# Kernel tuning notes

Hardware: AMD Instinct MI355X
Metric: run time of the kernel (lower is better)

The kernel has to match this reference:

```python
import jax, jax.numpy as jnp
import numpy as np

NS, NI, NC, C, E, M = 50000, 20000, 1000, 128, 1000000, 250000


def setup_inputs() -> dict:
    key = jax.random.key(0)
    ks = jax.random.split(key, 12)
    xavier = (2.0 / (C + C)) ** 0.5  # xavier_normal_ std for square weight
    return {
        "stu_x": jax.random.normal(ks[0], (NS, C), jnp.float32),
        "item_x": jax.random.normal(ks[1], (NI, C), jnp.float32),
        "conc_x": jax.random.normal(ks[2], (NC, C), jnp.float32),
        "W_stu": jax.random.normal(ks[3], (C, C), jnp.float32) * xavier,
        "b_stu": jnp.zeros((C,), jnp.float32),
        "W_item": jax.random.normal(ks[4], (C, C), jnp.float32) * xavier,
        "b_item": jnp.zeros((C,), jnp.float32),
        "W_pred": jax.random.normal(ks[5], (1, C), jnp.float32) * ((2.0 / (1 + C)) ** 0.5),
        "b_pred": jnp.zeros((1,), jnp.float32),
        "stu_track": jax.random.randint(ks[6], (E,), 0, NS, jnp.int32),
        "item_index": jax.random.randint(ks[7], (E,), 0, NI, jnp.int32),
        "conc_index": jax.random.randint(ks[8], (E,), 0, NC, jnp.int32),
        "mean_index": jax.random.randint(ks[9], (E,), 0, M, jnp.int32),
        "num_segments": M,
    }


def _segment_mean(vals, seg_ids, num_segments):
    sums = jax.ops.segment_sum(vals, seg_ids, num_segments=num_segments)
    cnt = jax.ops.segment_sum(jnp.ones((vals.shape[0], 1), vals.dtype), seg_ids,
                              num_segments=num_segments)
    return sums / jnp.maximum(cnt, 1.0)


def reference(stu_x, item_x, conc_x, W_stu, b_stu, W_item, b_item, W_pred, b_pred,
              stu_track, item_index, conc_index, mean_index, num_segments):
    # Feature (stu): shared lin_l=lin_r; aggregate is identity -> per-edge output
    conc_s = conc_x @ W_stu.T          # [NC, C] projected source (concepts)
    stu_p = stu_x @ W_stu.T            # [NS, C] projected target (students)
    stu_feature = jax.nn.sigmoid(conc_s[conc_index] + stu_p[stu_track] + b_stu)  # [E, C]

    # Feature (item): SparseTensor(row=item, col=conc) -> x_j from conc, x_i from item
    conc_i = conc_x @ W_item.T         # [NC, C]
    item_p = item_x @ W_item.T         # [NI, C]
    item_feature = jax.nn.sigmoid(conc_i[conc_index] + item_p[item_index] + b_item)  # [E, C]

    # scatter-mean of per-edge difference over mean_index groups
    pred_input = _segment_mean(stu_feature - item_feature, mean_index, num_segments)  # [M, C]
    pred = jax.nn.sigmoid(pred_input @ W_pred.T + b_pred)  # [M, 1]
    return pred.reshape(-1)
```

## Files before the change

kernel.cpp:

```cpp
#include <hip/hip_runtime.h>

typedef unsigned short u16;
typedef unsigned int   u32;

typedef short short8 __attribute__((ext_vector_type(8)));
typedef float floatx4 __attribute__((ext_vector_type(4)));

#define CDIM 128
#define K_NEG_LOG2E -1.4426950408889634f
#define CNT_SCALE 16777216.0

__device__ __forceinline__ float bf2f_lo(u32 h) {
    union { u32 u; float f; } v; v.u = h << 16; return v.f;
}
__device__ __forceinline__ float bf2f_hi(u32 h) {
    union { u32 u; float f; } v; v.u = h & 0xffff0000u; return v.f;
}
__device__ __forceinline__ u16 f2bf(float f) {
    union { float f; u32 u; } v; v.f = f;
    u32 u = v.u;
    return (u16)((u + 0x7FFFu + ((u >> 16) & 1u)) >> 16);
}
__device__ __forceinline__ float sig_std(float x) {
    return __builtin_amdgcn_rcpf(1.0f + __builtin_amdgcn_exp2f(x * K_NEG_LOG2E));
}

__global__ __launch_bounds__(256) void prep_kernel(
    const float* __restrict__ Wstu, const float* __restrict__ Witem,
    u32* __restrict__ Wbf_pair, float4* __restrict__ zero4, int nZero4)
{
    const int tid = blockIdx.x * blockDim.x + threadIdx.x;
    const int stride = gridDim.x * blockDim.x;
    for (int i = tid; i < 16384; i += stride) {
        const float* W = (i & 8192) ? (Witem - 16384) : Wstu;
        const int j = i * 2;
        u32 lo = f2bf(W[j]     * K_NEG_LOG2E);
        u32 hi = f2bf(W[j + 1] * K_NEG_LOG2E);
        Wbf_pair[i] = lo | (hi << 16);
    }
    const float4 z = {0.f, 0.f, 0.f, 0.f};
    for (int i = tid; i < nZero4; i += stride) zero4[i] = z;
}

__device__ __forceinline__ void proj_tile32(
    const float* __restrict__ X, const u16* __restrict__ Wbf,
    const float* __restrict__ bias, u16* __restrict__ out,
    int nrows, int ostride, int ooff, int row0, int lane)
{
    const int m = lane & 15;
    const int g = lane >> 4;

    short8 a[2][4];
#pragma unroll
    for (int t = 0; t < 2; ++t) {
        int arow = row0 + t * 16 + m;
        if (arow >= nrows) arow = nrows - 1;
        const float* xrow = X + (size_t)arow * CDIM;
#pragma unroll
        for (int s = 0; s < 4; ++s) {
            float4 f0 = *(const float4*)(xrow + s * 32 + g * 8);
            float4 f1 = *(const float4*)(xrow + s * 32 + g * 8 + 4);
            a[t][s][0] = (short)f2bf(f0.x); a[t][s][1] = (short)f2bf(f0.y);
            a[t][s][2] = (short)f2bf(f0.z); a[t][s][3] = (short)f2bf(f0.w);
            a[t][s][4] = (short)f2bf(f1.x); a[t][s][5] = (short)f2bf(f1.y);
            a[t][s][6] = (short)f2bf(f1.z); a[t][s][7] = (short)f2bf(f1.w);
        }
    }

#pragma unroll
    for (int ct = 0; ct < 8; ++ct) {
        const u16* wrow = Wbf + (size_t)(ct * 16 + m) * CDIM;
        floatx4 acc0 = {0.f, 0.f, 0.f, 0.f};
        floatx4 acc1 = {0.f, 0.f, 0.f, 0.f};
#pragma unroll
        for (int s = 0; s < 4; ++s) {
            short8 b = *(const short8*)(wrow + s * 32 + g * 8);
            acc0 = __builtin_amdgcn_mfma_f32_16x16x32_bf16(a[0][s], b, acc0, 0, 0, 0);
            acc1 = __builtin_amdgcn_mfma_f32_16x16x32_bf16(a[1][s], b, acc1, 0, 0, 0);
        }
        const int col = ct * 16 + m;
        const float badd = bias ? bias[col] * K_NEG_LOG2E : 0.f;
#pragma unroll
        for (int i = 0; i < 4; ++i) {
            int r0 = row0 + g * 4 + i;
            if (r0 < nrows)
                out[(size_t)r0 * ostride + ooff + col] =
                    f2bf(__builtin_amdgcn_exp2f(acc0[i] + badd));
            int r1 = r0 + 16;
            if (r1 < nrows)
                out[(size_t)r1 * ostride + ooff + col] =
                    f2bf(__builtin_amdgcn_exp2f(acc1[i] + badd));
        }
    }
}

__global__ __launch_bounds__(256) void proj4_kernel(
    const float* __restrict__ stu_x, const float* __restrict__ item_x,
    const float* __restrict__ conc_x,
    const u16* __restrict__ Wstu_bf, const u16* __restrict__ Witem_bf,
    const float* __restrict__ b_stu, const float* __restrict__ b_item,
    u16* __restrict__ stu_p, u16* __restrict__ item_p, u16* __restrict__ conc_cat,
    int NS, int NI, int NC)
{
    const int lane = threadIdx.x & 63;
    int w = blockIdx.x * 4 + (threadIdx.x >> 6);
    const int T0 = (NS + 31) / 32, T1 = (NI + 31) / 32, T2 = (NC + 31) / 32;

    if (w < T0) { proj_tile32(stu_x, Wstu_bf, nullptr, stu_p, NS, 128, 0, w * 32, lane); return; }
    w -= T0;
    if (w < T1) { proj_tile32(item_x, Witem_bf, nullptr, item_p, NI, 128, 0, w * 32, lane); return; }
    w -= T1;
    if (w < T2) { proj_tile32(conc_x, Wstu_bf, b_stu, conc_cat, NC, 256, 0, w * 32, lane); return; }
    w -= T2;
    if (w < T2) { proj_tile32(conc_x, Witem_bf, b_item, conc_cat, NC, 256, 128, w * 32, lane); return; }
}

__global__ __launch_bounds__(256) void edge_kernel(
    const u16* __restrict__ stu_p, const u16* __restrict__ item_p,
    const u16* __restrict__ conc_cat,
    const int* __restrict__ stu_track, const int* __restrict__ item_index,
    const int* __restrict__ conc_index, const int* __restrict__ mean_index,
    const float* __restrict__ w_pred,
    double* __restrict__ sc, int E)
{
    const int lane = threadIdx.x & 63;
    const int sub  = lane & 15;
    const int g    = lane >> 4;
    const int waveId = (int)((blockIdx.x * blockDim.x + threadIdx.x) >> 6);
    const int nWaves = (int)((gridDim.x * blockDim.x) >> 6);

    const float4 wA = ((const float4*)w_pred)[sub * 2];
    const float4 wB = ((const float4*)w_pred)[sub * 2 + 1];
    const float w8[8] = {wA.x, wA.y, wA.z, wA.w, wB.x, wB.y, wB.z, wB.w};
    const u32 lane_off = (u32)sub * 16;

    const int nQuads = (E + 3) >> 2;
    int q = waveId;
    if (q >= nQuads) return;

#define LOADIDX(qq, sN, iN, cN, mN, lN) { \
        int e_ = (qq) * 4 + g; int ec_ = (e_ < E) ? e_ : (E - 1); \
        lN = (e_ < E); \
        sN = stu_track[ec_]; iN = item_index[ec_]; \
        cN = conc_index[ec_]; mN = mean_index[ec_]; }

#define GATHER(si_, ii_, ci_, sv_, iv_, ca_, cb_) { \
        sv_ = *(const uint4*)((const char*)stu_p  + (((u32)(si_) << 8) + lane_off)); \
        iv_ = *(const uint4*)((const char*)item_p + (((u32)(ii_) << 8) + lane_off)); \
        const char* cp_ = (const char*)conc_cat + (((u32)(ci_) << 9) + lane_off); \
        ca_ = *(const uint4*)cp_; cb_ = *(const uint4*)(cp_ + 256); }

    int si, ii, ci, mi; bool live;
    LOADIDX(q, si, ii, ci, mi, live);
    uint4 sv, iv, ca, cb;
    GATHER(si, ii, ci, sv, iv, ca, cb);

    int qn = q + nWaves;
    bool more = (qn < nQuads);
    int si2 = 0, ii2 = 0, ci2 = 0, mi2 = 0; bool live2 = false;
    if (more) LOADIDX(qn, si2, ii2, ci2, mi2, live2);

    while (true) {
        uint4 svN, ivN, caN, cbN;
        if (more) GATHER(si2, ii2, ci2, svN, ivN, caN, cbN);

        const int qnn = qn + nWaves;
        const bool more2 = (qnn < nQuads);
        int si3 = 0, ii3 = 0, ci3 = 0, mi3 = 0; bool live3 = false;
        if (more2) LOADIDX(qnn, si3, ii3, ci3, mi3, live3);

        __builtin_amdgcn_sched_barrier(0);

        const u32 su[4] = {sv.x, sv.y, sv.z, sv.w};
        const u32 iu[4] = {iv.x, iv.y, iv.z, iv.w};
        const u32 au[4] = {ca.x, ca.y, ca.z, ca.w};
        const u32 bu[4] = {cb.x, cb.y, cb.z, cb.w};

        float v = 0.f;
#pragma unroll
        for (int j = 0; j < 4; ++j) {
            const float ea0 = bf2f_lo(au[j]) * bf2f_lo(su[j]);
            const float eb0 = bf2f_lo(bu[j]) * bf2f_lo(iu[j]);
            const float ea1 = bf2f_hi(au[j]) * bf2f_hi(su[j]);
            const float eb1 = bf2f_hi(bu[j]) * bf2f_hi(iu[j]);
            const float den0 = 1.0f + fmaf(ea0, eb0, ea0 + eb0);
            const float den1 = 1.0f + fmaf(ea1, eb1, ea1 + eb1);
            v += w8[2 * j]     * ((eb0 - ea0) * __builtin_amdgcn_rcpf(den0));
            v += w8[2 * j + 1] * ((eb1 - ea1) * __builtin_amdgcn_rcpf(den1));
        }

        v += __shfl_xor(v, 1, 64);
        v += __shfl_xor(v, 2, 64);
        v += __shfl_xor(v, 4, 64);
        v += __shfl_xor(v, 8, 64);

        if (sub == 0 && live) {
            atomicAdd(&sc[mi], (double)v + CNT_SCALE);
        }

        if (!more) break;
        sv = svN; iv = ivN; ca = caN; cb = cbN;
        mi = mi2; live = live2;
        q = qn; qn = qnn;
        si2 = si3; ii2 = ii3; ci2 = ci3; mi2 = mi3; live2 = live3;
        more = more2;
    }
#undef LOADIDX
#undef GATHER
}

__global__ __launch_bounds__(256) void final_kernel(
    const double* __restrict__ sc,
    const float* __restrict__ b_pred, float* __restrict__ out, int M)
{
    const int i = blockIdx.x * blockDim.x + threadIdx.x;
    if (i < M) {
        const double acc = sc[i];
        const double cnt = rint(acc * (1.0 / CNT_SCALE));
        const double sum = acc - cnt * CNT_SCALE;
        const float mean = (float)(sum / fmax(cnt, 1.0));
        out[i] = sig_std(mean + b_pred[0]);
    }
}

extern "C" void kernel_launch(void* const* d_in, const int* in_sizes, int n_in,
                              void* d_out, int out_size, void* d_ws, size_t ws_size,
                              hipStream_t stream) {
    const float* stu_x    = (const float*)d_in[0];
    const float* item_x   = (const float*)d_in[1];
    const float* conc_x   = (const float*)d_in[2];
    const float* W_stu    = (const float*)d_in[3];
    const float* b_stu    = (const float*)d_in[4];
    const float* W_item   = (const float*)d_in[5];
    const float* b_item   = (const float*)d_in[6];
    const float* W_pred   = (const float*)d_in[7];
    const float* b_pred   = (const float*)d_in[8];
    const int* stu_track  = (const int*)d_in[9];
    const int* item_index = (const int*)d_in[10];
    const int* conc_index = (const int*)d_in[11];
    const int* mean_index = (const int*)d_in[12];

    const int NS = in_sizes[0] / CDIM;
    const int NI = in_sizes[1] / CDIM;
    const int NC = in_sizes[2] / CDIM;
    const int E  = in_sizes[9];
    const int M  = out_size;

    double* sc     = (double*)d_ws;
    u16* Wstu_bf   = (u16*)(sc + M);
    u16* Witem_bf  = Wstu_bf + CDIM * CDIM;
    u16* stu_p     = Witem_bf + CDIM * CDIM;
    u16* item_p    = stu_p  + (size_t)NS * CDIM;
    u16* conc_cat  = item_p + (size_t)NI * CDIM;

    const int nZero4 = (int)(((size_t)M * sizeof(double)) / 16);
    prep_kernel<<<512, 256, 0, stream>>>(W_stu, W_item, (u32*)Wstu_bf,
                                         (float4*)sc, nZero4);

    const int T0 = (NS + 31) / 32, T1 = (NI + 31) / 32, T2 = (NC + 31) / 32;
    const int totalWaves = T0 + T1 + 2 * T2;
    proj4_kernel<<<(totalWaves + 3) / 4, 256, 0, stream>>>(
        stu_x, item_x, conc_x, Wstu_bf, Witem_bf, b_stu, b_item,
        stu_p, item_p, conc_cat, NS, NI, NC);

    edge_kernel<<<4096, 256, 0, stream>>>(stu_p, item_p, conc_cat,
                                          stu_track, item_index, conc_index, mean_index,
                                          W_pred, sc, E);

    final_kernel<<<(M + 255) / 256, 256, 0, stream>>>(sc, b_pred, (float*)d_out, M);
}
```

Before: 198.6 us.

## Pack pre-shifted edge indices into int4 and unroll edge pipeline by four

```diff
diff --git a/kernel.cpp b/kernel.cpp
--- a/kernel.cpp
+++ b/kernel.cpp
@@ -27,7 +27,10 @@
 
 __global__ __launch_bounds__(256) void prep_kernel(
     const float* __restrict__ Wstu, const float* __restrict__ Witem,
-    u32* __restrict__ Wbf_pair, float4* __restrict__ zero4, int nZero4)
+    u32* __restrict__ Wbf_pair, float4* __restrict__ zero4, int nZero4,
+    const int* __restrict__ stu_track, const int* __restrict__ item_index,
+    const int* __restrict__ conc_index, const int* __restrict__ mean_index,
+    int4* __restrict__ idx4, int E)
 {
     const int tid = blockIdx.x * blockDim.x + threadIdx.x;
     const int stride = gridDim.x * blockDim.x;
@@ -40,6 +43,14 @@
     }
     const float4 z = {0.f, 0.f, 0.f, 0.f};
     for (int i = tid; i < nZero4; i += stride) zero4[i] = z;
+    for (int e = tid; e < E; e += stride) {
+        int4 t;
+        t.x = stu_track[e]  << 8;
+        t.y = item_index[e] << 8;
+        t.z = conc_index[e] << 9;
+        t.w = mean_index[e] << 3;
+        idx4[e] = t;
+    }
 }
 
 __device__ __forceinline__ void proj_tile32(
@@ -118,8 +129,7 @@
 __global__ __launch_bounds__(256) void edge_kernel(
     const u16* __restrict__ stu_p, const u16* __restrict__ item_p,
     const u16* __restrict__ conc_cat,
-    const int* __restrict__ stu_track, const int* __restrict__ item_index,
-    const int* __restrict__ conc_index, const int* __restrict__ mean_index,
+    const int4* __restrict__ idx4,
     const float* __restrict__ w_pred,
     double* __restrict__ sc, int E)
 {
@@ -127,86 +137,82 @@
     const int sub  = lane & 15;
     const int g    = lane >> 4;
     const int waveId = (int)((blockIdx.x * blockDim.x + threadIdx.x) >> 6);
-    const int nWaves = (int)((gridDim.x * blockDim.x) >> 6);
+    const int S      = (int)((gridDim.x * blockDim.x) >> 6);
 
     const float4 wA = ((const float4*)w_pred)[sub * 2];
     const float4 wB = ((const float4*)w_pred)[sub * 2 + 1];
-    const float w8[8] = {wA.x, wA.y, wA.z, wA.w, wB.x, wB.y, wB.z, wB.w};
+    float2 w2[4];
+    w2[0] = make_float2(wA.x, wA.y); w2[1] = make_float2(wA.z, wA.w);
+    w2[2] = make_float2(wB.x, wB.y); w2[3] = make_float2(wB.z, wB.w);
     const u32 lane_off = (u32)sub * 16;
 
     const int nQuads = (E + 3) >> 2;
     int q = waveId;
     if (q >= nQuads) return;
 
-#define LOADIDX(qq, sN, iN, cN, mN, lN) { \
-        int e_ = (qq) * 4 + g; int ec_ = (e_ < E) ? e_ : (E - 1); \
-        lN = (e_ < E); \
-        sN = stu_track[ec_]; iN = item_index[ec_]; \
-        cN = conc_index[ec_]; mN = mean_index[ec_]; }
-
-#define GATHER(si_, ii_, ci_, sv_, iv_, ca_, cb_) { \
-        sv_ = *(const uint4*)((const char*)stu_p  + (((u32)(si_) << 8) + lane_off)); \
-        iv_ = *(const uint4*)((const char*)item_p + (((u32)(ii_) << 8) + lane_off)); \
-        const char* cp_ = (const char*)conc_cat + (((u32)(ci_) << 9) + lane_off); \
-        ca_ = *(const uint4*)cp_; cb_ = *(const uint4*)(cp_ + 256); }
-
-    int si, ii, ci, mi; bool live;
-    LOADIDX(q, si, ii, ci, mi, live);
-    uint4 sv, iv, ca, cb;
-    GATHER(si, ii, ci, sv, iv, ca, cb);
-
-    int qn = q + nWaves;
-    bool more = (qn < nQuads);
-    int si2 = 0, ii2 = 0, ci2 = 0, mi2 = 0; bool live2 = false;
-    if (more) LOADIDX(qn, si2, ii2, ci2, mi2, live2);
-
-    while (true) {
-        uint4 svN, ivN, caN, cbN;
-        if (more) GATHER(si2, ii2, ci2, svN, ivN, caN, cbN);
-
-        const int qnn = qn + nWaves;
-        const bool more2 = (qnn < nQuads);
-        int si3 = 0, ii3 = 0, ci3 = 0, mi3 = 0; bool live3 = false;
-        if (more2) LOADIDX(qnn, si3, ii3, ci3, mi3, live3);
-
-        __builtin_amdgcn_sched_barrier(0);
-
+    auto ldidx = [&](int qq) -> int4 {
+        int e = qq * 4 + g;
+        e = (e < E) ? e : (E - 1);
+        return idx4[e];
+    };
+    auto compute = [&](const uint4& sv, const uint4& iv,
+                       const uint4& ca, const uint4& cb,
+                       const int4& I, int qq) {
         const u32 su[4] = {sv.x, sv.y, sv.z, sv.w};
         const u32 iu[4] = {iv.x, iv.y, iv.z, iv.w};
         const u32 au[4] = {ca.x, ca.y, ca.z, ca.w};
         const u32 bu[4] = {cb.x, cb.y, cb.z, cb.w};
-
-        float v = 0.f;
+        const float2 one = make_float2(1.f, 1.f);
+        float2 vacc = make_float2(0.f, 0.f);
 #pragma unroll
         for (int j = 0; j < 4; ++j) {
-            const float ea0 = bf2f_lo(au[j]) * bf2f_lo(su[j]);
-            const float eb0 = bf2f_lo(bu[j]) * bf2f_lo(iu[j]);
-            const float ea1 = bf2f_hi(au[j]) * bf2f_hi(su[j]);
-            const float eb1 = bf2f_hi(bu[j]) * bf2f_hi(iu[j]);
-            const float den0 = 1.0f + fmaf(ea0, eb0, ea0 + eb0);
-            const float den1 = 1.0f + fmaf(ea1, eb1, ea1 + eb1);
-            v += w8[2 * j]     * ((eb0 - ea0) * __builtin_amdgcn_rcpf(den0));
-            v += w8[2 * j + 1] * ((eb1 - ea1) * __builtin_amdgcn_rcpf(den1));
-        }
-
+            float2 A  = make_float2(bf2f_lo(au[j]), bf2f_hi(au[j]));
+            float2 Sx = make_float2(bf2f_lo(su[j]), bf2f_hi(su[j]));
+            float2 B  = make_float2(bf2f_lo(bu[j]), bf2f_hi(bu[j]));
+            float2 Ix = make_float2(bf2f_lo(iu[j]), bf2f_hi(iu[j]));
+            float2 ea = A * Sx;
+            float2 eb = B * Ix;
+            float2 den = (ea + one) * (eb + one);
+            float2 num = eb - ea;
+            float2 rd = make_float2(__builtin_amdgcn_rcpf(den.x),
+                                    __builtin_amdgcn_rcpf(den.y));
+            vacc += (num * rd) * w2[j];
+        }
+        float v = vacc.x + vacc.y;
         v += __shfl_xor(v, 1, 64);
         v += __shfl_xor(v, 2, 64);
         v += __shfl_xor(v, 4, 64);
         v += __shfl_xor(v, 8, 64);
-
-        if (sub == 0 && live) {
-            atomicAdd(&sc[mi], (double)v + CNT_SCALE);
-        }
-
-        if (!more) break;
-        sv = svN; iv = ivN; ca = caN; cb = cbN;
-        mi = mi2; live = live2;
-        q = qn; qn = qnn;
-        si2 = si3; ii2 = ii3; ci2 = ci3; mi2 = mi3; live2 = live3;
-        more = more2;
-    }
-#undef LOADIDX
-#undef GATHER
+        if (sub == 0 && (qq * 4 + g) < E)
+            atomicAdd((double*)((char*)sc + (u32)I.w), (double)v + CNT_SCALE);
+    };
+
+#define GATH(I_, sv_, iv_, ca_, cb_) { \
+        sv_ = *(const uint4*)((const char*)stu_p  + ((u32)(I_).x + lane_off)); \
+        iv_ = *(const uint4*)((const char*)item_p + ((u32)(I_).y + lane_off)); \
+        const char* cp_ = (const char*)conc_cat + ((u32)(I_).z + lane_off); \
+        ca_ = *(const uint4*)cp_; cb_ = *(const uint4*)(cp_ + 256); }
+
+#define STEP(DA, DB, IA, IB, IC) { \
+        GATH(I##IB, sv##DB, iv##DB, ca##DB, cb##DB); \
+        I##IC = ldidx(q + 2 * S); \
+        __builtin_amdgcn_sched_barrier(0); \
+        compute(sv##DA, iv##DA, ca##DA, cb##DA, I##IA, q); \
+        q += S; \
+        if (q >= nQuads) break; }
+
+    int4 I0 = ldidx(q), I1 = ldidx(q + S), I2, I3;
+    uint4 sv0, iv0, ca0, cb0, sv1, iv1, ca1, cb1;
+    GATH(I0, sv0, iv0, ca0, cb0);
+
+    for (;;) {
+        STEP(0, 1, 0, 1, 2)
+        STEP(1, 0, 1, 2, 3)
+        STEP(0, 1, 2, 3, 0)
+        STEP(1, 0, 3, 0, 1)
+    }
+#undef STEP
+#undef GATH
 }
 
 __global__ __launch_bounds__(256) void final_kernel(
@@ -252,10 +258,13 @@
     u16* stu_p     = Witem_bf + CDIM * CDIM;
     u16* item_p    = stu_p  + (size_t)NS * CDIM;
     u16* conc_cat  = item_p + (size_t)NI * CDIM;
+    int4* idx4     = (int4*)(conc_cat + (size_t)NC * 256);
 
     const int nZero4 = (int)(((size_t)M * sizeof(double)) / 16);
-    prep_kernel<<<512, 256, 0, stream>>>(W_stu, W_item, (u32*)Wstu_bf,
-                                         (float4*)sc, nZero4);
+    prep_kernel<<<1024, 256, 0, stream>>>(W_stu, W_item, (u32*)Wstu_bf,
+                                          (float4*)sc, nZero4,
+                                          stu_track, item_index, conc_index,
+                                          mean_index, idx4, E);
 
     const int T0 = (NS + 31) / 32, T1 = (NI + 31) / 32, T2 = (NC + 31) / 32;
     const int totalWaves = T0 + T1 + 2 * T2;
@@ -264,8 +273,7 @@
         stu_p, item_p, conc_cat, NS, NI, NC);
 
     edge_kernel<<<4096, 256, 0, stream>>>(stu_p, item_p, conc_cat,
-                                          stu_track, item_index, conc_index, mean_index,
-                                          W_pred, sc, E);
+                                          idx4, W_pred, sc, E);
 
     final_kernel<<<(M + 255) / 256, 256, 0, stream>>>(sc, b_pred, (float*)d_out, M);
 }
```

Measured after the change: 196.7 us. About the same (-1.0%).
